# Performance work log

Hardware: AMD Instinct MI355X
Metric: run time of the kernel (lower is better)

Reference implementation:

```python
import jax, jax.numpy as jnp
import numpy as np

KERNEL_SIZE = 5
SIGMA_SPACE = 1.0
SIGMA_COLOR = 0.1
PAD = KERNEL_SIZE // 2


def make_spatial_kernel(kernel_size, sigma_space):
    r = kernel_size // 2
    coords = jnp.arange(-r, r + 1, dtype=jnp.float32)
    xx, yy = jnp.meshgrid(coords, coords, indexing='ij')
    return jnp.exp(-(xx ** 2 + yy ** 2) / (2.0 * sigma_space ** 2))  # [K, K]


def setup_inputs() -> dict:
    key = jax.random.key(0)
    x = jax.random.uniform(key, (4, 3, 512, 512), dtype=jnp.float32)
    spatial_kernel = make_spatial_kernel(KERNEL_SIZE, SIGMA_SPACE)
    sigma_color = jnp.float32(SIGMA_COLOR)
    return {"x": x, "spatial_kernel": spatial_kernel, "sigma_color": sigma_color}


def reference(x, spatial_kernel, sigma_color):
    # x: [B, C, H, W]; spatial_kernel: [K, K] (fixed buffer, computed at init)
    B, C, H, W = x.shape
    K = KERNEL_SIZE
    padded = jnp.pad(x, ((0, 0), (0, 0), (PAD, PAD), (PAD, PAD)), mode='reflect')
    # Gather KxK windows as a trailing tap axis: [B, C, H, W, K*K]
    patches = jnp.stack(
        [padded[:, :, i:i + H, j:j + W] for i in range(K) for j in range(K)],
        axis=-1,
    )
    sk = spatial_kernel.reshape(-1)  # [K*K]
    color_diff = patches - x[..., None]
    color_weight = jnp.exp(-(color_diff ** 2) / (2.0 * sigma_color ** 2))
    weight = sk * color_weight  # [B, C, H, W, K*K]
    weight = weight / (jnp.sum(weight, axis=-1, keepdims=True) + 1e-8)
    return jnp.sum(weight * patches, axis=-1)  # [B, C, H, W]
```

## Files before the change

### kernel.cpp

```cpp
#include <hip/hip_runtime.h>

constexpr int H = 512, W = 512;
constexpr int K = 5, PADR = 2;
constexpr int TR = 2;
constexpr int SR = TR + 4;

__device__ __forceinline__ float rfl(float v) {
    union { float f; int i; } u; u.f = v;
    u.i = __builtin_amdgcn_readfirstlane(u.i);
    return u.f;
}

constexpr int idx6(int d2) {
    return d2 == 0 ? 0 : d2 == 1 ? 1 : d2 == 2 ? 2 : d2 == 4 ? 3 : d2 == 5 ? 4 : 5;
}

__global__ __launch_bounds__(256, 4) void bilateral_kernel(
    const float* __restrict__ x,
    const float* __restrict__ sk,
    const float* __restrict__ sigma_color,
    float* __restrict__ out)
{
    __shared__ float lds[SR][W];

    int t = threadIdx.x;
    int wv = t >> 6;
    int l = t & 63;

    float lw[6];
    lw[0] = rfl(__builtin_amdgcn_logf(sk[12]));
    lw[1] = rfl(__builtin_amdgcn_logf(sk[7]));
    lw[2] = rfl(__builtin_amdgcn_logf(sk[6]));
    lw[3] = rfl(__builtin_amdgcn_logf(sk[2]));
    lw[4] = rfl(__builtin_amdgcn_logf(sk[1]));
    lw[5] = rfl(__builtin_amdgcn_logf(sk[0]));
    float sk12 = rfl(sk[12]);

    float s = sigma_color[0];
    float c2 = -1.4426950408889634f / (2.0f * s * s);

    int plane = blockIdx.x >> 8;
    int r0 = (blockIdx.x & 255) << 1;
    const float* xp = x + (size_t)plane * (H * W);

#pragma unroll
    for (int su = 0; su < 3; ++su) {
        int u = wv + (su << 2);
        int k = u >> 1, hh = u & 1;
        int gr = r0 - 2 + k;
        gr = (gr < 0) ? -gr : gr;
        gr = (gr >= H) ? (2 * H - 2 - gr) : gr;
        int col = (hh << 8) + (l << 2);
        float4 v = *(const float4*)(xp + (gr << 9) + col);
        *(float4*)(&lds[k][col]) = v;
    }
    __syncthreads();

    int rr = wv >> 1;
    int c  = ((wv & 1) << 6) + l;
    bool le = (c == 0), re = (c == 127);
    int cm1 = le ? 0   : c - 1;
    int cp1 = re ? 127 : c + 1;

    float cc[4], wsum[4], acc[4];
#pragma unroll
    for (int p = 0; p < 4; ++p) { wsum[p] = 0.f; acc[p] = 0.f; }

    constexpr int order[K] = {2, 0, 1, 3, 4};
#pragma unroll
    for (int oi = 0; oi < K; ++oi) {
        const int i = order[oi];
        const float* rp = &lds[rr + i][0];

        float4 a = *(const float4*)(rp + (cm1 << 2));
        float4 m = *(const float4*)(rp + (c   << 2));
        float4 b = *(const float4*)(rp + (cp1 << 2));

        float win[8];
        win[0] = le ? m.z : a.z;
        win[1] = le ? m.y : a.w;
        win[2] = m.x; win[3] = m.y; win[4] = m.z; win[5] = m.w;
        win[6] = re ? m.z : b.x;
        win[7] = re ? m.y : b.y;

        if (oi == 0) {
#pragma unroll
            for (int p = 0; p < 4; ++p) cc[p] = win[p + 2];
        }

#pragma unroll
        for (int j = 0; j < K; ++j) {
            if (i == 2 && j == 2) {
#pragma unroll
                for (int p = 0; p < 4; ++p) {
                    wsum[p] += sk12;
                    acc[p] = __builtin_fmaf(sk12, cc[p], acc[p]);
                }
            } else {
                const float lwv = lw[idx6((i - 2) * (i - 2) + (j - 2) * (j - 2))];
#pragma unroll
                for (int p = 0; p < 4; ++p) {
                    float v = win[p + j];
                    float d = v - cc[p];
                    float arg = __builtin_fmaf(d * c2, d, lwv);
                    float wq = __builtin_amdgcn_exp2f(arg);
                    wsum[p] += wq;
                    acc[p] = __builtin_fmaf(wq, v, acc[p]);
                }
            }
        }
    }

    float* op = out + (size_t)plane * (H * W) + ((size_t)(r0 + rr) << 9) + (c << 2);
    float4 o;
    o.x = acc[0] * __builtin_amdgcn_rcpf(wsum[0] + 1e-8f);
    o.y = acc[1] * __builtin_amdgcn_rcpf(wsum[1] + 1e-8f);
    o.z = acc[2] * __builtin_amdgcn_rcpf(wsum[2] + 1e-8f);
    o.w = acc[3] * __builtin_amdgcn_rcpf(wsum[3] + 1e-8f);
    *(float4*)op = o;
}

extern "C" void kernel_launch(void* const* d_in, const int* in_sizes, int n_in,
                              void* d_out, int out_size, void* d_ws, size_t ws_size,
                              hipStream_t stream) {
    const float* x  = (const float*)d_in[0];
    const float* sk = (const float*)d_in[1];
    const float* sc = (const float*)d_in[2];
    float* out = (float*)d_out;

    const int total = in_sizes[0];
    const int blocks = total / (256 * 4);
    bilateral_kernel<<<blocks, 256, 0, stream>>>(x, sk, sc, out);
}
```

Before: 82.17 us.

## Process four output rows per block and use packed float2 math

```diff
diff --git a/kernel.cpp b/kernel.cpp
--- a/kernel.cpp
+++ b/kernel.cpp
@@ -1,8 +1,10 @@
 #include <hip/hip_runtime.h>
 
+typedef float v2f __attribute__((ext_vector_type(2)));
+
 constexpr int H = 512, W = 512;
-constexpr int K = 5, PADR = 2;
-constexpr int TR = 2;
+constexpr int K = 5;
+constexpr int TR = 4;
 constexpr int SR = TR + 4;
 
 __device__ __forceinline__ float rfl(float v) {
@@ -38,86 +40,97 @@
 
     float s = sigma_color[0];
     float c2 = -1.4426950408889634f / (2.0f * s * s);
+    v2f c2v   = { c2, c2 };
+    v2f sk12v = { sk12, sk12 };
 
-    int plane = blockIdx.x >> 8;
-    int r0 = (blockIdx.x & 255) << 1;
+    int plane = blockIdx.x >> 7;
+    int r0 = (blockIdx.x & 127) << 2;
     const float* xp = x + (size_t)plane * (H * W);
+    float* outp = out + (size_t)plane * (H * W);
 
 #pragma unroll
-    for (int su = 0; su < 3; ++su) {
+    for (int su = 0; su < 4; ++su) {
         int u = wv + (su << 2);
         int k = u >> 1, hh = u & 1;
         int gr = r0 - 2 + k;
         gr = (gr < 0) ? -gr : gr;
         gr = (gr >= H) ? (2 * H - 2 - gr) : gr;
         int col = (hh << 8) + (l << 2);
-        float4 v = *(const float4*)(xp + (gr << 9) + col);
-        *(float4*)(&lds[k][col]) = v;
+        *(float4*)(&lds[k][col]) = *(const float4*)(xp + (gr << 9) + col);
     }
     __syncthreads();
 
-    int rr = wv >> 1;
-    int c  = ((wv & 1) << 6) + l;
-    bool le = (c == 0), re = (c == 127);
-    int cm1 = le ? 0   : c - 1;
-    int cp1 = re ? 127 : c + 1;
+#pragma unroll
+    for (int ti = 0; ti < 2; ++ti) {
+        int tk = wv + (ti << 2);
+        int rr = tk >> 1, hh = tk & 1;
+        int c  = (hh << 6) + l;
+        bool le = (c == 0), re = (c == 127);
+        int cm1 = le ? 0   : c - 1;
+        int cp1 = re ? 127 : c + 1;
 
-    float cc[4], wsum[4], acc[4];
+        v2f cc0, cc1, ws0, ws1, ac0, ac1;
+        ws0 = ws1 = ac0 = ac1 = (v2f){0.f, 0.f};
+        cc0 = cc1 = (v2f){0.f, 0.f};
+
+        constexpr int order[K] = {2, 0, 1, 3, 4};
 #pragma unroll
-    for (int p = 0; p < 4; ++p) { wsum[p] = 0.f; acc[p] = 0.f; }
+        for (int oi = 0; oi < K; ++oi) {
+            const int i = order[oi];
+            const float* rp = &lds[rr + i][0];
 
-    constexpr int order[K] = {2, 0, 1, 3, 4};
-#pragma unroll
-    for (int oi = 0; oi < K; ++oi) {
-        const int i = order[oi];
-        const float* rp = &lds[rr + i][0];
+            float4 a = *(const float4*)(rp + (cm1 << 2));
+            float4 m = *(const float4*)(rp + (c   << 2));
+            float4 b = *(const float4*)(rp + (cp1 << 2));
 
-        float4 a = *(const float4*)(rp + (cm1 << 2));
-        float4 m = *(const float4*)(rp + (c   << 2));
-        float4 b = *(const float4*)(rp + (cp1 << 2));
+            float win[8];
+            win[0] = le ? m.z : a.z;
+            win[1] = le ? m.y : a.w;
+            win[2] = m.x; win[3] = m.y; win[4] = m.z; win[5] = m.w;
+            win[6] = re ? m.z : b.x;
+            win[7] = re ? m.y : b.y;
 
-        float win[8];
-        win[0] = le ? m.z : a.z;
-        win[1] = le ? m.y : a.w;
-        win[2] = m.x; win[3] = m.y; win[4] = m.z; win[5] = m.w;
-        win[6] = re ? m.z : b.x;
-        win[7] = re ? m.y : b.y;
-
-        if (oi == 0) {
-#pragma unroll
-            for (int p = 0; p < 4; ++p) cc[p] = win[p + 2];
-        }
+            if (oi == 0) {
+                cc0 = (v2f){ win[2], win[3] };
+                cc1 = (v2f){ win[4], win[5] };
+            }
 
 #pragma unroll
-        for (int j = 0; j < K; ++j) {
-            if (i == 2 && j == 2) {
-#pragma unroll
-                for (int p = 0; p < 4; ++p) {
-                    wsum[p] += sk12;
-                    acc[p] = __builtin_fmaf(sk12, cc[p], acc[p]);
-                }
-            } else {
-                const float lwv = lw[idx6((i - 2) * (i - 2) + (j - 2) * (j - 2))];
-#pragma unroll
-                for (int p = 0; p < 4; ++p) {
-                    float v = win[p + j];
-                    float d = v - cc[p];
-                    float arg = __builtin_fmaf(d * c2, d, lwv);
-                    float wq = __builtin_amdgcn_exp2f(arg);
-                    wsum[p] += wq;
-                    acc[p] = __builtin_fmaf(wq, v, acc[p]);
+            for (int j = 0; j < K; ++j) {
+                if (i == 2 && j == 2) {
+                    ws0 += sk12v;
+                    ws1 += sk12v;
+                    ac0 = __builtin_elementwise_fma(sk12v, cc0, ac0);
+                    ac1 = __builtin_elementwise_fma(sk12v, cc1, ac1);
+                } else {
+                    const float lwv = lw[idx6((i - 2) * (i - 2) + (j - 2) * (j - 2))];
+                    v2f lsp = { lwv, lwv };
+                    v2f v0 = { win[j],     win[j + 1] };
+                    v2f v1 = { win[j + 2], win[j + 3] };
+                    v2f d0 = v0 - cc0;
+                    v2f d1 = v1 - cc1;
+                    v2f g0 = __builtin_elementwise_fma(d0 * c2v, d0, lsp);
+                    v2f g1 = __builtin_elementwise_fma(d1 * c2v, d1, lsp);
+                    v2f w0, w1;
+                    w0[0] = __builtin_amdgcn_exp2f(g0[0]);
+                    w0[1] = __builtin_amdgcn_exp2f(g0[1]);
+                    w1[0] = __builtin_amdgcn_exp2f(g1[0]);
+                    w1[1] = __builtin_amdgcn_exp2f(g1[1]);
+                    ws0 += w0;
+                    ws1 += w1;
+                    ac0 = __builtin_elementwise_fma(w0, v0, ac0);
+                    ac1 = __builtin_elementwise_fma(w1, v1, ac1);
                 }
             }
         }
+
+        float4 o;
+        o.x = ac0[0] * __builtin_amdgcn_rcpf(ws0[0] + 1e-8f);
+        o.y = ac0[1] * __builtin_amdgcn_rcpf(ws0[1] + 1e-8f);
+        o.z = ac1[0] * __builtin_amdgcn_rcpf(ws1[0] + 1e-8f);
+        o.w = ac1[1] * __builtin_amdgcn_rcpf(ws1[1] + 1e-8f);
+        *(float4*)(outp + ((size_t)(r0 + rr) << 9) + (c << 2)) = o;
     }
-
-    float* op = out + (size_t)plane * (H * W) + ((size_t)(r0 + rr) << 9) + (c << 2);
-    float4 o;
-    o.x = acc[0] * __builtin_amdgcn_rcpf(wsum[0] + 1e-8f);
-    o.y = acc[1] * __builtin_amdgcn_rcpf(wsum[1] + 1e-8f);
-    o.z = acc[2] * __builtin_amdgcn_rcpf(wsum[2] + 1e-8f);
-    o.w = acc[3] * __builtin_amdgcn_rcpf(wsum[3] + 1e-8f);
-    *(float4*)op = o;
 }
 
 extern "C" void kernel_launch(void* const* d_in, const int* in_sizes, int n_in,
@@ -129,6 +142,6 @@
     float* out = (float*)d_out;
 
     const int total = in_sizes[0];
-    const int blocks = total / (256 * 4);
+    const int blocks = total / (256 * 8);
     bilateral_kernel<<<blocks, 256, 0, stream>>>(x, sk, sc, out);
 }
```

New measurement: 77.10 us. 6.2% less time.
